# Optimization experiments

Hardware: AMD Instinct MI355X
Metric: run time of the kernel (lower is better)

The kernel has to match this reference:

```python
import jax, jax.numpy as jnp
import numpy as np

N = 50000
E = 800000
F_IN = 256
HID = 64
HEADS = 4
CLASSES = 32
NEG_SLOPE = 0.2


def setup_inputs() -> dict:
    key = jax.random.key(0)
    ks = jax.random.split(key, 10)
    x = jax.random.normal(ks[0], (N, F_IN), dtype=jnp.float32)
    edge_index = jax.random.randint(ks[1], (2, E), 0, N, dtype=jnp.int64)
    s1 = 1.0 / np.sqrt(F_IN)
    s2 = 1.0 / np.sqrt(HID * HEADS)
    W1 = jax.random.normal(ks[2], (F_IN, HEADS * HID), dtype=jnp.float32) * s1
    a_src1 = jax.random.normal(ks[3], (HEADS, HID), dtype=jnp.float32) * s1
    a_dst1 = jax.random.normal(ks[4], (HEADS, HID), dtype=jnp.float32) * s1
    b1 = jnp.zeros((HEADS * HID,), dtype=jnp.float32)
    W2 = jax.random.normal(ks[5], (HEADS * HID, CLASSES), dtype=jnp.float32) * s2
    a_src2 = jax.random.normal(ks[6], (1, CLASSES), dtype=jnp.float32) * s2
    a_dst2 = jax.random.normal(ks[7], (1, CLASSES), dtype=jnp.float32) * s2
    b2 = jnp.zeros((CLASSES,), dtype=jnp.float32)
    return {"x": x, "edge_index": edge_index, "W1": W1, "a_src1": a_src1,
            "a_dst1": a_dst1, "b1": b1, "W2": W2, "a_src2": a_src2,
            "a_dst2": a_dst2, "b2": b2}


def gat_conv(x, src, dst, W, a_src, a_dst, bias, num_nodes):
    # PyG GATConv: h = x W, per-head attention logits, segment softmax over dst,
    # scatter-weighted aggregation. src/dst already include self-loops.
    H, C = a_src.shape
    h = (x @ W).reshape(num_nodes, H, C)               # [N, H, C]
    al_s = jnp.sum(h * a_src[None], axis=-1)            # [N, H]
    al_d = jnp.sum(h * a_dst[None], axis=-1)            # [N, H]
    e = jax.nn.leaky_relu(al_s[src] + al_d[dst], NEG_SLOPE)  # [Et, H]
    m = jax.ops.segment_max(e, dst, num_segments=num_nodes)  # [N, H]
    ex = jnp.exp(e - m[dst])
    denom = jax.ops.segment_sum(ex, dst, num_segments=num_nodes)
    alpha = ex / denom[dst]                              # [Et, H]
    out = jax.ops.segment_sum(alpha[:, :, None] * h[src], dst,
                              num_segments=num_nodes)    # [N, H, C]
    return out.reshape(num_nodes, H * C) + bias


def reference(x, edge_index, W1, a_src1, a_dst1, b1, W2, a_src2, a_dst2, b2):
    num_nodes = x.shape[0]
    loop = jnp.arange(num_nodes, dtype=edge_index.dtype)
    src = jnp.concatenate([edge_index[0], loop])  # add_self_loops=True (PyG default)
    dst = jnp.concatenate([edge_index[1], loop])
    # dropout is identity in eval mode
    h = jax.nn.elu(gat_conv(x, src, dst, W1, a_src1, a_dst1, b1, num_nodes))
    out = gat_conv(h, src, dst, W2, a_src2, a_dst2, b2, num_nodes)
    return jax.nn.log_softmax(out, axis=1)
```

## Files before the change

kernel.cpp:

```cpp
#include <hip/hip_runtime.h>
#include <math.h>

#define N_NODES 50000
#define N_EDGES 800000
#define NEG_SLOPE 0.2f
#define PADU N_NODES
#define LOG2E 1.44269504088896f

#define BSHIFT 8
#define NBUK ((N_NODES + 255) >> BSHIFT)
#define BCAP 4608
#define ACHUNK 4096
#define ET_PAD_ALLOC 1000960

typedef __attribute__((ext_vector_type(8))) short s16x8;
typedef __attribute__((ext_vector_type(4))) float f32x4;
typedef __attribute__((ext_vector_type(2))) float f32x2;

__device__ __forceinline__ unsigned short f2bf(float f) {
    union { float f; unsigned u; } v; v.f = f;
    unsigned r = v.u + 0x7FFF + ((v.u >> 16) & 1);
    return (unsigned short)(r >> 16);
}
__device__ __forceinline__ float asf(unsigned u) {
    union { unsigned u; float f; } v; v.u = u;
    return v.f;
}
__device__ __forceinline__ uint4 pack_bf16_trunc(float4 f0, float4 f1) {
    const unsigned* a = (const unsigned*)&f0;
    const unsigned* b = (const unsigned*)&f1;
    uint4 r;
    r.x = (a[0] >> 16) | (a[1] & 0xffff0000u);
    r.y = (a[2] >> 16) | (a[3] & 0xffff0000u);
    r.z = (b[0] >> 16) | (b[1] & 0xffff0000u);
    r.w = (b[2] >> 16) | (b[3] & 0xffff0000u);
    return r;
}
__device__ __forceinline__ unsigned char f2fp8(float f) {
    return (unsigned char)(__builtin_amdgcn_cvt_pk_fp8_f32(f, f, 0, false) & 0xff);
}


__global__ __launch_bounds__(256) void k_cvtw(const float* __restrict__ W1, const float* __restrict__ W2,
                                              unsigned short* __restrict__ WT, unsigned short* __restrict__ W2T,
                                              int* __restrict__ bcur, float* __restrict__ als1,
                                              unsigned char* __restrict__ H8) {
    int b = blockIdx.x, k = threadIdx.x;
    if (b < 256) {
        WT[b * 256 + k] = f2bf(W1[k * 256 + b]);
    } else if (b < 288) {
        int c = b - 256;
        W2T[c * 256 + k] = f2bf(W2[k * 32 + c]);
    } else {
        if (k < NBUK) bcur[k] = 0;
        if (k >= 196 && k < 200) als1[N_NODES * 4 + (k - 196)] = -1e30f;
        if (k >= 200 && k < 264) ((unsigned*)(H8 + (size_t)N_NODES * 256))[k - 200] = 0;
    }
}


__global__ __launch_bounds__(256) void k_bin(const int* __restrict__ ei, int* __restrict__ bcur,
                                             unsigned* __restrict__ stage) {
    __shared__ unsigned sdata[ACHUNK];
    __shared__ unsigned short sv[ACHUNK];
    __shared__ int scnt[NBUK];
    __shared__ int soff[NBUK + 1];
    __shared__ int sgbase[NBUK];
    __shared__ int wssc[4];
    int tid = threadIdx.x;
    int e0 = blockIdx.x * ACHUNK;
    int nE = N_EDGES - e0;
    if (nE > ACHUNK) nE = ACHUNK;
    for (int i = tid; i < NBUK; i += 256) scnt[i] = 0;
    __syncthreads();
    for (int i = tid; i < nE; i += 256) {
        int v = ei[N_EDGES + e0 + i];
        sv[i] = (unsigned short)v;
        atomicAdd(&scnt[v >> BSHIFT], 1);
    }
    __syncthreads();
    {
        int lane = tid & 63, w = tid >> 6;
        int val = (tid < NBUK) ? scnt[tid] : 0;
        int incl = val;
        for (int o = 1; o < 64; o <<= 1) {
            int t = __shfl_up(incl, o);
            if (lane >= o) incl += t;
        }
        if (lane == 63) wssc[w] = incl;
        __syncthreads();
        int wb = 0;
        for (int i = 0; i < w; ++i) wb += wssc[i];
        if (tid < NBUK) soff[tid] = wb + incl - val;
        if (tid == 255) soff[NBUK] = wb + incl;
    }
    __syncthreads();
    if (tid < NBUK) {
        int c = scnt[tid];
        sgbase[tid] = c ? atomicAdd(&bcur[tid], c) : 0;
        scnt[tid] = soff[tid];
    }
    __syncthreads();
    for (int i = tid; i < nE; i += 256) {
        int u = ei[e0 + i];
        unsigned v = sv[i];
        int b = (int)(v >> BSHIFT);
        int pos = atomicAdd(&scnt[b], 1);
        sdata[pos] = (unsigned)u | ((v & 255u) << 16) | ((unsigned)b << 24);
    }
    __syncthreads();
    for (int i = tid; i < nE; i += 256) {
        unsigned pk = sdata[i];
        int buk = (int)(pk >> 24);
        int rel = sgbase[buk] + (i - soff[buk]);
        if (rel < BCAP) stage[(size_t)buk * BCAP + rel] = pk;
    }
}


__global__ __launch_bounds__(256) void k_bukscan(const int* __restrict__ bcur, int* __restrict__ bukbase) {
    __shared__ int ws[4];
    int tid = threadIdx.x, lane = tid & 63, w = tid >> 6;
    int val = 0;
    if (tid < NBUK) {
        int base = tid << BSHIFT;
        int nv = N_NODES - base;
        if (nv > 256) nv = 256;
        val = (bcur[tid] + 4 * nv + 3) & ~3;
    }
    int incl = val;
    for (int o = 1; o < 64; o <<= 1) {
        int t = __shfl_up(incl, o);
        if (lane >= o) incl += t;
    }
    if (lane == 63) ws[w] = incl;
    __syncthreads();
    int wb = 0;
    for (int i = 0; i < w; ++i) wb += ws[i];
    if (tid < NBUK) bukbase[tid] = wb + incl - val;
}


__global__ __launch_bounds__(256) void k_build(const unsigned* __restrict__ stage,
                                               const int* __restrict__ bcur, const int* __restrict__ bukbase,
                                               int* __restrict__ offp, int* __restrict__ ecnt,
                                               unsigned short* __restrict__ esrc) {
    __shared__ int hist[256];
    __shared__ int lexcl[257];
    __shared__ int ws[4];
    __shared__ int outbuf[5632];
    int b = blockIdx.x, tid = threadIdx.x;
    int n = bcur[b];
    if (n > BCAP) n = BCAP;
    int base = b << BSHIFT;
    int nv = N_NODES - base;
    if (nv > 256) nv = 256;
    hist[tid] = 0;
    __syncthreads();
    const unsigned* sg = stage + (size_t)b * BCAP;
    for (int i = tid; i < n; i += 256) atomicAdd(&hist[(sg[i] >> 16) & 0xFF], 1);
    __syncthreads();
    int lane = tid & 63, w = tid >> 6;
    int c = (tid < nv) ? hist[tid] + 1 : 0;
    int r = (tid < nv) ? ((c + 3) & ~3) : 0;
    int incl = r;
    for (int o = 1; o < 64; o <<= 1) {
        int t = __shfl_up(incl, o);
        if (lane >= o) incl += t;
    }
    if (lane == 63) ws[w] = incl;
    __syncthreads();
    int wb = 0;
    for (int i = 0; i < w; ++i) wb += ws[i];
    int excl = wb + incl - r;
    lexcl[tid] = excl;
    if (tid == 255) lexcl[256] = excl + r;
    int gb = bukbase[b];
    if (tid < nv) {
        offp[base + tid] = gb + excl;
        ecnt[base + tid] = c;
    }
    __syncthreads();
    int total = lexcl[256];
    if (tid < nv) {
        outbuf[excl] = base + tid;
        for (int j = excl + c; j < excl + r; ++j) outbuf[j] = PADU;
        hist[tid] = 1;
    }
    __syncthreads();
    for (int i = tid; i < n; i += 256) {
        unsigned pk = sg[i];
        int vloc = (int)((pk >> 16) & 0xFF);
        int pos = lexcl[vloc] + atomicAdd(&hist[vloc], 1);
        outbuf[pos] = (int)(pk & 0xffffu);
    }
    __syncthreads();
    for (int i = tid; i < total; i += 256) esrc[gb + i] = (unsigned short)outbuf[i];
}


__global__ __launch_bounds__(256) void k_gemm1m(const float* __restrict__ X, const unsigned short* __restrict__ WT,
                                                const float* __restrict__ a_src, const float* __restrict__ a_dst,
                                                unsigned char* __restrict__ H8,
                                                float* __restrict__ als, float* __restrict__ ald) {
    __shared__ unsigned short As[64][40];
    __shared__ unsigned short Bs[256][40];
    int tid = threadIdx.x;
    int row0 = blockIdx.x * 64;
    int wv = tid >> 6, lane = tid & 63;
    int wm = wv & 1, wn = wv >> 1;
    int lr = lane & 15, quad = lane >> 4;
    f32x4 acc[2][8];
#pragma unroll
    for (int mt = 0; mt < 2; ++mt)
#pragma unroll
        for (int nt = 0; nt < 8; ++nt) acc[mt][nt] = (f32x4){0.f, 0.f, 0.f, 0.f};

    int ar = tid >> 2, aseg = tid & 3;
    for (int k0 = 0; k0 < 256; k0 += 32) {
        {
            int grow = row0 + ar;
            float4 f0 = make_float4(0.f, 0.f, 0.f, 0.f), f1 = f0;
            if (grow < N_NODES) {
                const float* src = X + (size_t)grow * 256 + k0 + aseg * 8;
                f0 = *(const float4*)src;
                f1 = *(const float4*)(src + 4);
            }
            *(uint4*)&As[ar][aseg * 8] = pack_bf16_trunc(f0, f1);
        }
#pragma unroll
        for (int pass = 0; pass < 4; ++pass) {
            int q = tid + pass * 256;
            int n = q >> 2, seg = q & 3;
            uint4 v = *(const uint4*)(WT + (n << 8) + k0 + seg * 8);
            *(uint4*)&Bs[n][seg * 8] = v;
        }
        __syncthreads();
        s16x8 a[2], b[8];
#pragma unroll
        for (int mt = 0; mt < 2; ++mt) a[mt] = *(const s16x8*)&As[wm * 32 + mt * 16 + lr][quad * 8];
#pragma unroll
        for (int nt = 0; nt < 8; ++nt) b[nt] = *(const s16x8*)&Bs[wn * 128 + nt * 16 + lr][quad * 8];
#pragma unroll
        for (int mt = 0; mt < 2; ++mt)
#pragma unroll
            for (int nt = 0; nt < 8; ++nt)
                acc[mt][nt] = __builtin_amdgcn_mfma_f32_16x16x32_bf16(a[mt], b[nt], acc[mt][nt], 0, 0, 0);
        __syncthreads();
    }
#pragma unroll
    for (int mt = 0; mt < 2; ++mt) {
#pragma unroll
        for (int r = 0; r < 4; ++r) {
            int row = row0 + wm * 32 + mt * 16 + quad * 4 + r;
            if (row < N_NODES) {
#pragma unroll
                for (int nt = 0; nt < 8; ++nt) {
                    int col = wn * 128 + nt * 16 + lr;
                    H8[(size_t)row * 256 + col] = f2fp8(acc[mt][nt][r]);
                }
            }
        }
    }
    float av[8], dv[8];
#pragma unroll
    for (int nt = 0; nt < 8; ++nt) {
        int col = wn * 128 + nt * 16 + lr;
        av[nt] = a_src[col] * LOG2E;
        dv[nt] = a_dst[col] * LOG2E;
    }
    float ps[2][8], pd[2][8];
#pragma unroll
    for (int hl = 0; hl < 2; ++hl)
#pragma unroll
        for (int i = 0; i < 8; ++i) { ps[hl][i] = 0.f; pd[hl][i] = 0.f; }
#pragma unroll
    for (int mt = 0; mt < 2; ++mt)
#pragma unroll
        for (int nt = 0; nt < 8; ++nt) {
            int hl = nt >> 2;
#pragma unroll
            for (int r = 0; r < 4; ++r) {
                float v = acc[mt][nt][r];
                ps[hl][mt * 4 + r] = fmaf(v, av[nt], ps[hl][mt * 4 + r]);
                pd[hl][mt * 4 + r] = fmaf(v, dv[nt], pd[hl][mt * 4 + r]);
            }
        }
#pragma unroll
    for (int hl = 0; hl < 2; ++hl)
#pragma unroll
        for (int i = 0; i < 8; ++i) {
            float s = ps[hl][i], d = pd[hl][i];
#pragma unroll
            for (int m = 8; m >= 1; m >>= 1) { s += __shfl_xor(s, m); d += __shfl_xor(d, m); }
            if (lr == 0) {
                int row = row0 + wm * 32 + (i >> 2) * 16 + quad * 4 + (i & 3);
                if (row < N_NODES) {
                    als[row * 4 + wn * 2 + hl] = s;
                    ald[row * 4 + wn * 2 + hl] = d;
                }
            }
        }
}


__global__ __launch_bounds__(256) void k_agg1(const unsigned* __restrict__ H8u,
                                              const float* __restrict__ als, const float* __restrict__ ald_,
                                              const int* __restrict__ offp, const int* __restrict__ ecnt,
                                              const unsigned short* __restrict__ esrc,
                                              const float* __restrict__ b1, unsigned* __restrict__ H2p) {
    int wid = (blockIdx.x * 256 + threadIdx.x) >> 6;
    int lane = threadIdx.x & 63;
    int head = lane >> 4;
    float ald = ald_[wid * 4 + head];
    int pstart = offp[wid];
    int rend = pstart + ((ecnt[wid] + 3) & ~3);
    float l = 0.f;
    f32x2 axy = (f32x2){0.f, 0.f}, azw = (f32x2){0.f, 0.f};

    auto quad = [&](unsigned ua, unsigned ub) {
        int u0 = (int)(ua & 0xffffu), u1 = (int)(ua >> 16);
        int u2 = (int)(ub & 0xffffu), u3 = (int)(ub >> 16);
        unsigned v0 = H8u[(unsigned)u0 * 64 + lane];
        unsigned v1 = H8u[(unsigned)u1 * 64 + lane];
        unsigned v2 = H8u[(unsigned)u2 * 64 + lane];
        unsigned v3 = H8u[(unsigned)u3 * 64 + lane];
        f32x2 e01 = (f32x2){als[u0 * 4 + head], als[u1 * 4 + head]} + (f32x2){ald, ald};
        f32x2 e23 = (f32x2){als[u2 * 4 + head], als[u3 * 4 + head]} + (f32x2){ald, ald};
        f32x2 t01 = e01 * NEG_SLOPE, t23 = e23 * NEG_SLOPE;
        float e0 = fmaxf(e01.x, t01.x), e1 = fmaxf(e01.y, t01.y);
        float e2 = fmaxf(e23.x, t23.x), e3 = fmaxf(e23.y, t23.y);
        float pw0 = __builtin_amdgcn_exp2f(e0);
        float pw1 = __builtin_amdgcn_exp2f(e1);
        float pw2 = __builtin_amdgcn_exp2f(e2);
        float pw3 = __builtin_amdgcn_exp2f(e3);
        l += (pw0 + pw1) + (pw2 + pw3);
        f32x2 a0 = __builtin_amdgcn_cvt_pk_f32_fp8(v0, false), b0 = __builtin_amdgcn_cvt_pk_f32_fp8(v0, true);
        f32x2 a1 = __builtin_amdgcn_cvt_pk_f32_fp8(v1, false), b1v = __builtin_amdgcn_cvt_pk_f32_fp8(v1, true);
        f32x2 a2 = __builtin_amdgcn_cvt_pk_f32_fp8(v2, false), b2v = __builtin_amdgcn_cvt_pk_f32_fp8(v2, true);
        f32x2 a3 = __builtin_amdgcn_cvt_pk_f32_fp8(v3, false), b3v = __builtin_amdgcn_cvt_pk_f32_fp8(v3, true);
        axy += (f32x2){pw0, pw0} * a0;
        azw += (f32x2){pw0, pw0} * b0;
        axy += (f32x2){pw1, pw1} * a1;
        azw += (f32x2){pw1, pw1} * b1v;
        axy += (f32x2){pw2, pw2} * a2;
        azw += (f32x2){pw2, pw2} * b2v;
        axy += (f32x2){pw3, pw3} * a3;
        azw += (f32x2){pw3, pw3} * b3v;
    };

    int p = pstart;
    for (; p + 7 < rend; p += 8) {
        uint2 ua = *(const uint2*)(esrc + p);
        uint2 ub = *(const uint2*)(esrc + p + 4);
        quad(ua.x, ua.y);
        quad(ub.x, ub.y);
    }
    if (p < rend) {
        uint2 ua = *(const uint2*)(esrc + p);
        quad(ua.x, ua.y);
    }

    float inv = 1.f / l;
    int c = lane * 4;
    float4 bb = *(const float4*)(b1 + c);
    float o0 = axy.x * inv + bb.x, o1 = axy.y * inv + bb.y, o2 = azw.x * inv + bb.z, o3 = azw.y * inv + bb.w;
    o0 = o0 > 0.f ? o0 : expm1f(o0);
    o1 = o1 > 0.f ? o1 : expm1f(o1);
    o2 = o2 > 0.f ? o2 : expm1f(o2);
    o3 = o3 > 0.f ? o3 : expm1f(o3);
    unsigned pk = __builtin_amdgcn_cvt_pk_fp8_f32(o0, o1, 0, false);
    pk = __builtin_amdgcn_cvt_pk_fp8_f32(o2, o3, pk, true);
    H2p[(unsigned)wid * 64 + lane] = pk;
}


__global__ __launch_bounds__(256) void k_gemm2m(const unsigned* __restrict__ H2p,
                                                const unsigned short* __restrict__ W2T,
                                                const float* __restrict__ as2, const float* __restrict__ ad2,
                                                unsigned short* __restrict__ Gb, float* __restrict__ als2,
                                                float* __restrict__ ald2) {
    int tid = threadIdx.x;
    int wv = tid >> 6, lane = tid & 63, lr = lane & 15, quad = lane >> 4;
    int row0 = blockIdx.x * 64 + wv * 16;
    int rowA = row0 + lr;
    unsigned rA = (rowA < N_NODES) ? (unsigned)rowA : (unsigned)(N_NODES - 1);
    f32x4 acc[2];
    acc[0] = (f32x4){0.f, 0.f, 0.f, 0.f};
    acc[1] = (f32x4){0.f, 0.f, 0.f, 0.f};
#pragma unroll
    for (int k0 = 0; k0 < 256; k0 += 32) {
        uint2 d = *(const uint2*)(H2p + rA * 64 + (k0 >> 2) + quad * 2);
        f32x2 f0 = __builtin_amdgcn_cvt_pk_f32_fp8(d.x, false);
        f32x2 f1 = __builtin_amdgcn_cvt_pk_f32_fp8(d.x, true);
        f32x2 f2 = __builtin_amdgcn_cvt_pk_f32_fp8(d.y, false);
        f32x2 f3 = __builtin_amdgcn_cvt_pk_f32_fp8(d.y, true);
        union { uint4 u; s16x8 s; } cv;
        cv.u = pack_bf16_trunc(make_float4(f0.x, f0.y, f1.x, f1.y), make_float4(f2.x, f2.y, f3.x, f3.y));
        s16x8 afrag = cv.s;
        s16x8 b0 = *(const s16x8*)(W2T + lr * 256 + k0 + quad * 8);
        s16x8 b1f = *(const s16x8*)(W2T + (16 + lr) * 256 + k0 + quad * 8);
        acc[0] = __builtin_amdgcn_mfma_f32_16x16x32_bf16(afrag, b0, acc[0], 0, 0, 0);
        acc[1] = __builtin_amdgcn_mfma_f32_16x16x32_bf16(afrag, b1f, acc[1], 0, 0, 0);
    }
    float a2s = as2[lr] * LOG2E, a2s2 = as2[16 + lr] * LOG2E;
    float a2d = ad2[lr] * LOG2E, a2d2 = ad2[16 + lr] * LOG2E;
#pragma unroll
    for (int r = 0; r < 4; ++r) {
        int row = row0 + quad * 4 + r;
        float g0 = acc[0][r], g1 = acc[1][r];
        float s = g0 * a2s + g1 * a2s2;
        float dd = g0 * a2d + g1 * a2d2;
#pragma unroll
        for (int m = 8; m >= 1; m >>= 1) { s += __shfl_xor(s, m); dd += __shfl_xor(dd, m); }
        if (row < N_NODES) {
            Gb[(size_t)row * 32 + lr] = f2bf(g0);
            Gb[(size_t)row * 32 + 16 + lr] = f2bf(g1);
            if (lr == 0) { als2[row] = s; ald2[row] = dd; }
        }
    }
}


__global__ __launch_bounds__(256) void k_agg2(const unsigned short* __restrict__ Gb,
                                              const float* __restrict__ als2,
                                              const float* __restrict__ ald2_, const int* __restrict__ offp,
                                              const int* __restrict__ ecnt,
                                              const unsigned short* __restrict__ esrc, const float* __restrict__ b2,
                                              float* __restrict__ out) {
    int gid = blockIdx.x * 256 + threadIdx.x;
    int node = gid >> 4;
    int colp = gid & 15;
    if (node >= N_NODES) return;
    float ald = ald2_[node];
    int pstart = offp[node];
    int pend = pstart + ecnt[node];
    float l = 0.f;
    f32x2 accv = (f32x2){0.f, 0.f};

    auto edge1 = [&](int u0) {
        unsigned gpk = *(const unsigned*)(Gb + (size_t)(unsigned)u0 * 32 + 2 * colp);
        f32x2 g01 = (f32x2){asf(gpk << 16), asf(gpk & 0xffff0000u)};
        float e0 = als2[u0] + ald;
        e0 = fmaxf(e0, NEG_SLOPE * e0);
        float pw0 = __builtin_amdgcn_exp2f(e0);
        l += pw0;
        accv += (f32x2){pw0, pw0} * g01;
    };
    auto quad = [&](unsigned ua, unsigned ub) {
        int u0 = (int)(ua & 0xffffu), u1 = (int)(ua >> 16);
        int u2 = (int)(ub & 0xffffu), u3 = (int)(ub >> 16);
        unsigned g0p = *(const unsigned*)(Gb + (size_t)(unsigned)u0 * 32 + 2 * colp);
        unsigned g1p = *(const unsigned*)(Gb + (size_t)(unsigned)u1 * 32 + 2 * colp);
        unsigned g2p = *(const unsigned*)(Gb + (size_t)(unsigned)u2 * 32 + 2 * colp);
        unsigned g3p = *(const unsigned*)(Gb + (size_t)(unsigned)u3 * 32 + 2 * colp);
        f32x2 e01 = (f32x2){als2[u0], als2[u1]} + (f32x2){ald, ald};
        f32x2 e23 = (f32x2){als2[u2], als2[u3]} + (f32x2){ald, ald};
        f32x2 t01 = e01 * NEG_SLOPE, t23 = e23 * NEG_SLOPE;
        float e0 = fmaxf(e01.x, t01.x), e1 = fmaxf(e01.y, t01.y);
        float e2 = fmaxf(e23.x, t23.x), e3 = fmaxf(e23.y, t23.y);
        float pw0 = __builtin_amdgcn_exp2f(e0), pw1 = __builtin_amdgcn_exp2f(e1);
        float pw2 = __builtin_amdgcn_exp2f(e2), pw3 = __builtin_amdgcn_exp2f(e3);
        l += (pw0 + pw1) + (pw2 + pw3);
        f32x2 g0 = (f32x2){asf(g0p << 16), asf(g0p & 0xffff0000u)};
        f32x2 g1 = (f32x2){asf(g1p << 16), asf(g1p & 0xffff0000u)};
        f32x2 g2 = (f32x2){asf(g2p << 16), asf(g2p & 0xffff0000u)};
        f32x2 g3 = (f32x2){asf(g3p << 16), asf(g3p & 0xffff0000u)};
        accv += (f32x2){pw0, pw0} * g0;
        accv += (f32x2){pw1, pw1} * g1;
        accv += (f32x2){pw2, pw2} * g2;
        accv += (f32x2){pw3, pw3} * g3;
    };

    int p = pstart;
    for (; p + 7 < pend; p += 8) {
        uint2 ua = *(const uint2*)(esrc + p);
        uint2 ub = *(const uint2*)(esrc + p + 4);
        quad(ua.x, ua.y);
        quad(ub.x, ub.y);
    }
    for (; p + 3 < pend; p += 4) {
        uint2 ua = *(const uint2*)(esrc + p);
        quad(ua.x, ua.y);
    }
    for (; p < pend; ++p) edge1(esrc[p]);

    float inv = 1.f / l;
    float2 bb = *(const float2*)(b2 + 2 * colp);
    float o0 = accv.x * inv + bb.x;
    float o1 = accv.y * inv + bb.y;
    float mm = fmaxf(o0, o1);
#pragma unroll
    for (int msk = 8; msk >= 1; msk >>= 1) mm = fmaxf(mm, __shfl_xor(mm, msk));
    float s = __expf(o0 - mm) + __expf(o1 - mm);
#pragma unroll
    for (int msk = 8; msk >= 1; msk >>= 1) s += __shfl_xor(s, msk);
    float ls = logf(s);
    float2 res = make_float2(o0 - mm - ls, o1 - mm - ls);
    *(float2*)(out + (size_t)node * 32 + 2 * colp) = res;
}


extern "C" void kernel_launch(void* const* d_in, const int* in_sizes, int n_in,
                              void* d_out, int out_size, void* d_ws, size_t ws_size,
                              hipStream_t stream) {
    const float* x   = (const float*)d_in[0];
    const int*   ei  = (const int*)d_in[1];
    const float* W1  = (const float*)d_in[2];
    const float* as1 = (const float*)d_in[3];
    const float* ad1 = (const float*)d_in[4];
    const float* b1  = (const float*)d_in[5];
    const float* W2  = (const float*)d_in[6];
    const float* as2 = (const float*)d_in[7];
    const float* ad2 = (const float*)d_in[8];
    const float* b2  = (const float*)d_in[9];
    float* out = (float*)d_out;

    char* p = (char*)d_ws;
    auto alloc = [&](size_t bytes) {
        char* r = p;
        p += (bytes + 255) & ~(size_t)255;
        return r;
    };
    unsigned char*  h8  = (unsigned char*)alloc((size_t)(N_NODES + 1) * 256);
    unsigned char*  h2pr= (unsigned char*)alloc((size_t)N_NODES * 64 * 4);
    unsigned short* wt  = (unsigned short*)alloc((size_t)256 * 256 * 2);
    unsigned short* w2t = (unsigned short*)alloc((size_t)32 * 256 * 2);
    float* als1 = (float*)alloc(((size_t)N_NODES * 4 + 4) * 4);
    float* ald1 = (float*)alloc((size_t)N_NODES * 4 * 4);
    float* als2 = (float*)alloc((size_t)N_NODES * 4);
    float* ald2 = (float*)alloc((size_t)N_NODES * 4);
    int* bcur    = (int*)alloc(256 * 4);
    int* bukbase = (int*)alloc(256 * 4);
    int* offp = (int*)alloc((size_t)N_NODES * 4);
    int* ecnt = (int*)alloc((size_t)N_NODES * 4);
    unsigned short* esrc = (unsigned short*)alloc((size_t)ET_PAD_ALLOC * 2);

    unsigned* stage = (unsigned*)h2pr;
    unsigned* h2p = (unsigned*)h2pr;
    unsigned short* g = (unsigned short*)h8;

    k_cvtw<<<289, 256, 0, stream>>>(W1, W2, wt, w2t, bcur, als1, h8);
    k_bin<<<(N_EDGES + ACHUNK - 1) / ACHUNK, 256, 0, stream>>>(ei, bcur, stage);
    k_bukscan<<<1, 256, 0, stream>>>(bcur, bukbase);
    k_build<<<NBUK, 256, 0, stream>>>(stage, bcur, bukbase, offp, ecnt, esrc);

    k_gemm1m<<<(N_NODES + 63) / 64, 256, 0, stream>>>(x, wt, as1, ad1, h8, als1, ald1);
    k_agg1<<<N_NODES / 4, 256, 0, stream>>>((const unsigned*)h8, als1, ald1, offp, ecnt, esrc, b1, h2p);
    k_gemm2m<<<(N_NODES + 63) / 64, 256, 0, stream>>>(h2p, w2t, as2, ad2, g, als2, ald2);
    k_agg2<<<(N_NODES * 16 + 255) / 256, 256, 0, stream>>>(g, als2, ald2, offp, ecnt, esrc, b2, out);
}
```

Measured before the change: 222.9 us.

## Split layer-1 features into per-head planes and drop bucket scan kernel

The fp8 hidden features from the first GEMM are now stored as four per-head planes of 64 bytes per node. Each aggregation block handles one head for 16 nodes, so gathers from neighbour rows hit a smaller per-head working set that should sit better in cache. Separately, the single-block bucket prefix-scan kernel is removed by giving every bucket a fixed padded slot in the edge array, which trades extra memory for one fewer launch. The ordering of blocks across heads changes how warps share edge lists, so the edge index and attention-logit reads are now repeated once per head.

New measurement: 227.9 us. 1.02x slower.

```diff
diff --git a/kernel.cpp b/kernel.cpp
--- a/kernel.cpp
+++ b/kernel.cpp
@@ -11,7 +11,8 @@
 #define NBUK ((N_NODES + 255) >> BSHIFT)
 #define BCAP 4608
 #define ACHUNK 4096
-#define ET_PAD_ALLOC 1000960
+#define PADBUK 5632
+#define ET_PAD_ALLOC (NBUK * PADBUK)
 
 typedef __attribute__((ext_vector_type(8))) short s16x8;
 typedef __attribute__((ext_vector_type(4))) float f32x4;
@@ -54,7 +55,11 @@
     } else {
         if (k < NBUK) bcur[k] = 0;
         if (k >= 196 && k < 200) als1[N_NODES * 4 + (k - 196)] = -1e30f;
-        if (k >= 200 && k < 264) ((unsigned*)(H8 + (size_t)N_NODES * 256))[k - 200] = 0;
+        if (k >= 200 && k < 264) {
+            int w = k - 200;
+            int plane = w >> 4, wi = w & 15;
+            ((unsigned*)H8)[((size_t)plane * (N_NODES + 1) + N_NODES) * 16 + wi] = 0;
+        }
     }
 }
 
@@ -118,37 +123,14 @@
 }
 
 
-__global__ __launch_bounds__(256) void k_bukscan(const int* __restrict__ bcur, int* __restrict__ bukbase) {
-    __shared__ int ws[4];
-    int tid = threadIdx.x, lane = tid & 63, w = tid >> 6;
-    int val = 0;
-    if (tid < NBUK) {
-        int base = tid << BSHIFT;
-        int nv = N_NODES - base;
-        if (nv > 256) nv = 256;
-        val = (bcur[tid] + 4 * nv + 3) & ~3;
-    }
-    int incl = val;
-    for (int o = 1; o < 64; o <<= 1) {
-        int t = __shfl_up(incl, o);
-        if (lane >= o) incl += t;
-    }
-    if (lane == 63) ws[w] = incl;
-    __syncthreads();
-    int wb = 0;
-    for (int i = 0; i < w; ++i) wb += ws[i];
-    if (tid < NBUK) bukbase[tid] = wb + incl - val;
-}
-
-
 __global__ __launch_bounds__(256) void k_build(const unsigned* __restrict__ stage,
-                                               const int* __restrict__ bcur, const int* __restrict__ bukbase,
+                                               const int* __restrict__ bcur,
                                                int* __restrict__ offp, int* __restrict__ ecnt,
                                                unsigned short* __restrict__ esrc) {
     __shared__ int hist[256];
     __shared__ int lexcl[257];
     __shared__ int ws[4];
-    __shared__ int outbuf[5632];
+    __shared__ int outbuf[PADBUK];
     int b = blockIdx.x, tid = threadIdx.x;
     int n = bcur[b];
     if (n > BCAP) n = BCAP;
@@ -175,7 +157,7 @@
     int excl = wb + incl - r;
     lexcl[tid] = excl;
     if (tid == 255) lexcl[256] = excl + r;
-    int gb = bukbase[b];
+    int gb = b * PADBUK;
     if (tid < nv) {
         offp[base + tid] = gb + excl;
         ecnt[base + tid] = c;
@@ -257,7 +239,8 @@
 #pragma unroll
                 for (int nt = 0; nt < 8; ++nt) {
                     int col = wn * 128 + nt * 16 + lr;
-                    H8[(size_t)row * 256 + col] = f2fp8(acc[mt][nt][r]);
+                    int plane = col >> 6;
+                    H8[((size_t)plane * (N_NODES + 1) + row) * 64 + (col & 63)] = f2fp8(acc[mt][nt][r]);
                 }
             }
         }
@@ -309,22 +292,24 @@
                                               const int* __restrict__ offp, const int* __restrict__ ecnt,
                                               const unsigned short* __restrict__ esrc,
                                               const float* __restrict__ b1, unsigned* __restrict__ H2p) {
-    int wid = (blockIdx.x * 256 + threadIdx.x) >> 6;
-    int lane = threadIdx.x & 63;
-    int head = lane >> 4;
-    float ald = ald_[wid * 4 + head];
-    int pstart = offp[wid];
-    int rend = pstart + ((ecnt[wid] + 3) & ~3);
+    int tid = threadIdx.x;
+    int head = blockIdx.x & 3;
+    int node = (blockIdx.x >> 2) * 16 + (tid >> 4);
+    int lane16 = tid & 15;
+    const unsigned* Hp = H8u + (size_t)head * (N_NODES + 1) * 16;
+    float ald = ald_[node * 4 + head];
+    int pstart = offp[node];
+    int rend = pstart + ((ecnt[node] + 3) & ~3);
     float l = 0.f;
     f32x2 axy = (f32x2){0.f, 0.f}, azw = (f32x2){0.f, 0.f};
 
     auto quad = [&](unsigned ua, unsigned ub) {
         int u0 = (int)(ua & 0xffffu), u1 = (int)(ua >> 16);
         int u2 = (int)(ub & 0xffffu), u3 = (int)(ub >> 16);
-        unsigned v0 = H8u[(unsigned)u0 * 64 + lane];
-        unsigned v1 = H8u[(unsigned)u1 * 64 + lane];
-        unsigned v2 = H8u[(unsigned)u2 * 64 + lane];
-        unsigned v3 = H8u[(unsigned)u3 * 64 + lane];
+        unsigned v0 = Hp[(unsigned)u0 * 16 + lane16];
+        unsigned v1 = Hp[(unsigned)u1 * 16 + lane16];
+        unsigned v2 = Hp[(unsigned)u2 * 16 + lane16];
+        unsigned v3 = Hp[(unsigned)u3 * 16 + lane16];
         f32x2 e01 = (f32x2){als[u0 * 4 + head], als[u1 * 4 + head]} + (f32x2){ald, ald};
         f32x2 e23 = (f32x2){als[u2 * 4 + head], als[u3 * 4 + head]} + (f32x2){ald, ald};
         f32x2 t01 = e01 * NEG_SLOPE, t23 = e23 * NEG_SLOPE;
@@ -362,8 +347,8 @@
     }
 
     float inv = 1.f / l;
-    int c = lane * 4;
-    float4 bb = *(const float4*)(b1 + c);
+    int ell = head * 16 + lane16;
+    float4 bb = *(const float4*)(b1 + ell * 4);
     float o0 = axy.x * inv + bb.x, o1 = axy.y * inv + bb.y, o2 = azw.x * inv + bb.z, o3 = azw.y * inv + bb.w;
     o0 = o0 > 0.f ? o0 : expm1f(o0);
     o1 = o1 > 0.f ? o1 : expm1f(o1);
@@ -371,7 +356,7 @@
     o3 = o3 > 0.f ? o3 : expm1f(o3);
     unsigned pk = __builtin_amdgcn_cvt_pk_fp8_f32(o0, o1, 0, false);
     pk = __builtin_amdgcn_cvt_pk_fp8_f32(o2, o3, pk, true);
-    H2p[(unsigned)wid * 64 + lane] = pk;
+    H2p[(unsigned)node * 64 + ell] = pk;
 }
 
 
@@ -531,7 +516,6 @@
     float* als2 = (float*)alloc((size_t)N_NODES * 4);
     float* ald2 = (float*)alloc((size_t)N_NODES * 4);
     int* bcur    = (int*)alloc(256 * 4);
-    int* bukbase = (int*)alloc(256 * 4);
     int* offp = (int*)alloc((size_t)N_NODES * 4);
     int* ecnt = (int*)alloc((size_t)N_NODES * 4);
     unsigned short* esrc = (unsigned short*)alloc((size_t)ET_PAD_ALLOC * 2);
@@ -542,11 +526,10 @@
 
     k_cvtw<<<289, 256, 0, stream>>>(W1, W2, wt, w2t, bcur, als1, h8);
     k_bin<<<(N_EDGES + ACHUNK - 1) / ACHUNK, 256, 0, stream>>>(ei, bcur, stage);
-    k_bukscan<<<1, 256, 0, stream>>>(bcur, bukbase);
-    k_build<<<NBUK, 256, 0, stream>>>(stage, bcur, bukbase, offp, ecnt, esrc);
+    k_build<<<NBUK, 256, 0, stream>>>(stage, bcur, offp, ecnt, esrc);
 
     k_gemm1m<<<(N_NODES + 63) / 64, 256, 0, stream>>>(x, wt, as1, ad1, h8, als1, ald1);
-    k_agg1<<<N_NODES / 4, 256, 0, stream>>>((const unsigned*)h8, als1, ald1, offp, ecnt, esrc, b1, h2p);
+    k_agg1<<<(N_NODES / 16) * 4, 256, 0, stream>>>((const unsigned*)h8, als1, ald1, offp, ecnt, esrc, b1, h2p);
     k_gemm2m<<<(N_NODES + 63) / 64, 256, 0, stream>>>(h2p, w2t, as2, ad2, g, als2, ald2);
     k_agg2<<<(N_NODES * 16 + 255) / 256, 256, 0, stream>>>(g, als2, ald2, offp, ecnt, esrc, b2, out);
 }
```
